# Optimization experiments

Measured on AMD Instinct MI355X. Metric: run time of the kernel, lower is better.

## Reference

```python
import jax, jax.numpy as jnp
import numpy as np

N, E, F_IN = 50000, 800000, 64
H, C1, C2 = 4, 32, 64
NUM_GRAPHS, NUM_CLASSES = 128, 8
NEG_SLOPE = 0.2


def _glorot(key, shape):
    fan_in, fan_out = shape[1], shape[0]
    lim = (6.0 / (fan_in + fan_out)) ** 0.5
    return jax.random.uniform(key, shape, jnp.float32, -lim, lim)


def setup_inputs() -> dict:
    key = jax.random.key(0)
    ks = jax.random.split(key, 20)
    x = jax.random.normal(ks[0], (N, F_IN), jnp.float32)
    edge_index = jax.random.randint(ks[1], (2, E), 0, N, jnp.int64)
    batch = jnp.sort(jax.random.randint(ks[2], (N,), 0, NUM_GRAPHS, jnp.int64))
    d1, d2 = H * C1, H * C2
    return {
        "x": x, "edge_index": edge_index, "batch": batch,
        # GATv2 layer 1 (F_IN -> 32, 4 heads)
        "Wl1": _glorot(ks[3], (d1, F_IN)), "bl1": jnp.zeros((d1,), jnp.float32),
        "Wr1": _glorot(ks[4], (d1, F_IN)), "br1": jnp.zeros((d1,), jnp.float32),
        "att1": _glorot(ks[5], (H, C1)), "bias1": jnp.zeros((d1,), jnp.float32),
        # GATv2 layer 2 (128 -> 64, 4 heads)
        "Wl2": _glorot(ks[6], (d2, d1)), "bl2": jnp.zeros((d2,), jnp.float32),
        "Wr2": _glorot(ks[7], (d2, d1)), "br2": jnp.zeros((d2,), jnp.float32),
        "att2": _glorot(ks[8], (H, C2)), "bias2": jnp.zeros((d2,), jnp.float32),
        # classifier: Linear(256,128) -> ReLU -> (Dropout eval=id) -> Linear(128,8)
        "Wf1": _glorot(ks[9], (128, d2)), "bf1": jnp.zeros((128,), jnp.float32),
        "Wf2": _glorot(ks[10], (NUM_CLASSES, 128)), "bf2": jnp.zeros((NUM_CLASSES,), jnp.float32),
    }


def _gatv2(x, src, dst, Wl, bl, Wr, br, att, bias, heads, out_ch):
    # PyG GATv2Conv: xl = lin_l(x) (source), xr = lin_r(x) (target)
    xl = (x @ Wl.T + bl).reshape(N, heads, out_ch)
    xr = (x @ Wr.T + br).reshape(N, heads, out_ch)
    # per-edge score: att . LeakyReLU(xl[j] + xr[i])  -> [E', H]
    e = jnp.sum(jax.nn.leaky_relu(xl[src] + xr[dst], NEG_SLOPE) * att, axis=-1)
    # destination-grouped softmax (self-loops guarantee every node has an edge)
    emax = jax.ops.segment_max(e, dst, num_segments=N)
    ex = jnp.exp(e - emax[dst])
    denom = jax.ops.segment_sum(ex, dst, num_segments=N)
    alpha = ex / denom[dst]  # [E', H]
    out = jax.ops.segment_sum(alpha[:, :, None] * xl[src], dst, num_segments=N)
    return out.reshape(N, heads * out_ch) + bias


def reference(x, edge_index, batch, Wl1, bl1, Wr1, br1, att1, bias1,
              Wl2, bl2, Wr2, br2, att2, bias2, Wf1, bf1, Wf2, bf2):
    # add self loops (PyG default add_self_loops=True)
    loops = jnp.arange(N, dtype=edge_index.dtype)
    src = jnp.concatenate([edge_index[0], loops])
    dst = jnp.concatenate([edge_index[1], loops])
    h = jax.nn.elu(_gatv2(x, src, dst, Wl1, bl1, Wr1, br1, att1, bias1, H, C1))
    h = jax.nn.elu(_gatv2(h, src, dst, Wl2, bl2, Wr2, br2, att2, bias2, H, C2))
    # global mean pool over graphs
    sums = jax.ops.segment_sum(h, batch, num_segments=NUM_GRAPHS)
    cnts = jax.ops.segment_sum(jnp.ones((N,), h.dtype), batch, num_segments=NUM_GRAPHS)
    pooled = sums / jnp.maximum(cnts, 1.0)[:, None]  # [G, 256]
    # classifier (dropout inactive at inference)
    z = jax.nn.relu(pooled @ Wf1.T + bf1)
    return z @ Wf2.T + bf2
```

## Files before the change

kernel.cpp:

```cpp
#include <hip/hip_runtime.h>
#include <hip/hip_bf16.h>
#include <math.h>

#define NN 50000
#define NE 800000
#define NEP (NE + NN)
#define NG 128
#define PSPLIT 16
#define NSB ((NN + 255) / 256)

typedef unsigned short u16;
typedef __bf16 bf16x8 __attribute__((ext_vector_type(8)));
typedef float f32x4 __attribute__((ext_vector_type(4)));

#define L2E 1.4426950408889634f

__device__ __forceinline__ float eluf(float v) {
  return v > 0.0f ? v : expm1f(v);
}
__device__ __forceinline__ float bflo(unsigned u) {
  union { unsigned i; float f; } c; c.i = u << 16; return c.f;
}
__device__ __forceinline__ float bfhi(unsigned u) {
  union { unsigned i; float f; } c; c.i = u & 0xffff0000u; return c.f;
}
__device__ __forceinline__ bf16x8 load8(const u16* p) {
  union { uint4 u; bf16x8 v; } c;
  c.u = *(const uint4*)p;
  return c.v;
}

__global__ __launch_bounds__(256) void k_deg(const int* __restrict__ ei, int* __restrict__ deg) {
  int t = blockIdx.x * 256 + threadIdx.x;
  if (t >= NEP) return;
  int dst = (t < NE) ? ei[NE + t] : (t - NE);
  atomicAdd(&deg[dst], 1);
}

__global__ __launch_bounds__(256) void k_scan1(const int* __restrict__ deg, int* __restrict__ bsum) {
  __shared__ int red[256];
  int i = blockIdx.x * 256 + threadIdx.x;
  red[threadIdx.x] = (i < NN) ? deg[i] : 0;
  __syncthreads();
  for (int off = 128; off > 0; off >>= 1) {
    if (threadIdx.x < off) red[threadIdx.x] += red[threadIdx.x + off];
    __syncthreads();
  }
  if (threadIdx.x == 0) bsum[blockIdx.x] = red[0];
}

__global__ __launch_bounds__(256) void k_scan2(int* __restrict__ bsum) {
  __shared__ int s[256];
  int t = threadIdx.x;
  s[t] = (t < NSB) ? bsum[t] : 0;
  __syncthreads();
  for (int off = 1; off < 256; off <<= 1) {
    int v = (t >= off) ? s[t - off] : 0;
    __syncthreads();
    s[t] += v;
    __syncthreads();
  }
  if (t < NSB) bsum[t] = (t == 0) ? 0 : s[t - 1];
}

__global__ __launch_bounds__(256) void k_scan3(const int* __restrict__ deg, const int* __restrict__ bsum,
                                               int* __restrict__ rowptr) {
  __shared__ int s[256];
  int t = threadIdx.x;
  int i = blockIdx.x * 256 + t;
  s[t] = (i < NN) ? deg[i] : 0;
  __syncthreads();
  for (int off = 1; off < 256; off <<= 1) {
    int v = (t >= off) ? s[t - off] : 0;
    __syncthreads();
    s[t] += v;
    __syncthreads();
  }
  int excl = (t == 0) ? 0 : s[t - 1];
  if (i <= NN) rowptr[i] = bsum[blockIdx.x] + excl;
}

__global__ __launch_bounds__(256) void k_scatter(const int* __restrict__ ei, const int* __restrict__ rowptr,
                                                 int* __restrict__ fill, int* __restrict__ srcidx) {
  int t = blockIdx.x * 256 + threadIdx.x;
  if (t >= NEP) return;
  int src, dst;
  if (t < NE) { src = ei[t]; dst = ei[NE + t]; } else { src = t - NE; dst = src; }
  int pos = atomicAdd(&fill[dst], 1);
  srcidx[rowptr[dst] + pos] = src;
}

__global__ __launch_bounds__(256) void k_cvtw(const float* __restrict__ w1, const float* __restrict__ w2,
                                              const float* __restrict__ w3, const float* __restrict__ w4,
                                              u16* __restrict__ o) {
  int t = blockIdx.x * 256 + threadIdx.x;
  if (t >= 81920) return;
  float v;
  if (t < 8192) v = w1[t];
  else if (t < 16384) v = w2[t - 8192];
  else if (t < 49152) v = w3[t - 16384];
  else v = w4[t - 49152];
  __hip_bfloat16 b = __float2bfloat16(v);
  o[t] = *(u16*)&b;
}

template <int K, bool AF32>
__global__ __launch_bounds__(256) void k_mfma(const void* __restrict__ Xin,
                                              const u16* __restrict__ Wlb, const u16* __restrict__ Wrb,
                                              const float* __restrict__ bl, const float* __restrict__ br,
                                              __hip_bfloat16* __restrict__ Yl, float* __restrict__ Yr,
                                              int dout) {
  int lane = threadIdx.x & 63;
  int wid = threadIdx.x >> 6;
  int r0 = blockIdx.x * 64 + wid * 16;
  int c0 = blockIdx.y * 64;
  bool isR = (blockIdx.z != 0);
  const u16* W = isR ? Wrb : Wlb;
  const float* bias = isR ? br : bl;

  int arow = min(r0 + (lane & 15), NN - 1);
  int koff = (lane >> 4) * 8;
  const u16*   aph = (const u16*)Xin + (size_t)arow * K + koff;
  const float* apf = (const float*)Xin + (size_t)arow * K + koff;
  const u16* bp = W + (size_t)(c0 + (lane & 15)) * K + koff;

  f32x4 acc[4] = {};
#pragma unroll
  for (int ks = 0; ks < K / 32; ++ks) {
    bf16x8 a;
    if constexpr (AF32) {
      float4 f0 = ((const float4*)(apf + ks * 32))[0];
      float4 f1 = ((const float4*)(apf + ks * 32))[1];
      a[0] = (__bf16)f0.x; a[1] = (__bf16)f0.y; a[2] = (__bf16)f0.z; a[3] = (__bf16)f0.w;
      a[4] = (__bf16)f1.x; a[5] = (__bf16)f1.y; a[6] = (__bf16)f1.z; a[7] = (__bf16)f1.w;
    } else {
      a = load8(aph + ks * 32);
    }
    bf16x8 b0 = load8(bp + ks * 32);
    bf16x8 b1 = load8(bp + 16 * K + ks * 32);
    bf16x8 b2 = load8(bp + 32 * K + ks * 32);
    bf16x8 b3 = load8(bp + 48 * K + ks * 32);
    acc[0] = __builtin_amdgcn_mfma_f32_16x16x32_bf16(a, b0, acc[0], 0, 0, 0);
    acc[1] = __builtin_amdgcn_mfma_f32_16x16x32_bf16(a, b1, acc[1], 0, 0, 0);
    acc[2] = __builtin_amdgcn_mfma_f32_16x16x32_bf16(a, b2, acc[2], 0, 0, 0);
    acc[3] = __builtin_amdgcn_mfma_f32_16x16x32_bf16(a, b3, acc[3], 0, 0, 0);
  }

  int orow = r0 + ((lane >> 4) << 2);
  int ocol = c0 + (lane & 15);
#pragma unroll
  for (int t = 0; t < 4; ++t) {
    int col = ocol + t * 16;
    float bv = bias[col];
    if (!isR) {
#pragma unroll
      for (int v = 0; v < 4; ++v) {
        int row = orow + v;
        if (row < NN) Yl[(size_t)row * dout + col] = __float2bfloat16(acc[t][v] + bv);
      }
    } else {
#pragma unroll
      for (int v = 0; v < 4; ++v) {
        int row = orow + v;
        if (row < NN) Yr[(size_t)row * dout + col] = acc[t][v] + bv;
      }
    }
  }
}

template <int D, bool OBF16>
__global__ __launch_bounds__(256) void k_fused(const int* __restrict__ rowptr, const int* __restrict__ srcidx,
                                               const u16* __restrict__ xl, const float* __restrict__ xr,
                                               const float* __restrict__ att, const float* __restrict__ bias,
                                               void* __restrict__ outv) {
  constexpr int V = D / 64;
  constexpr int SH = (V == 2) ? 8 : 9;
  int lane = threadIdx.x & 63;
  int node = blockIdx.x * 4 + (threadIdx.x >> 6);
  if (node >= NN) return;
  int lo = rowptr[node], hi = rowptr[node + 1];

  float xrv[V], attv[V];
  float rlin = 0.f;
#pragma unroll
  for (int q = 0; q < V; ++q) {
    attv[q] = att[lane * V + q] * (0.4f * L2E);
    xrv[q]  = xr[(size_t)node * D + lane * V + q];
    rlin = fmaf(attv[q], xrv[q], rlin);
  }
#pragma unroll
  for (int off = 1; off < 16; off <<= 1) rlin += __shfl_xor(rlin, off);
  float S0 = 1.5f * rlin;

  const char* xb = (const char*)xl;
  unsigned lb = (unsigned)lane << (SH - 6);

  float denom = 0.f;
  float acc[V] = {};

  auto gather = [&](int j, float* xv) {
    unsigned off = ((unsigned)j << SH) + lb;
    if constexpr (V == 2) {
      unsigned u = *(const unsigned*)(xb + off);
      xv[0] = bflo(u); xv[1] = bfhi(u);
    } else {
      uint2 u = *(const uint2*)(xb + off);
      xv[0] = bflo(u.x); xv[1] = bfhi(u.x);
      xv[2] = bflo(u.y); xv[3] = bfhi(u.y);
    }
  };
  auto score2 = [&](const float* xv) {
    float pa = 0.f, pl = 0.f;
#pragma unroll
    for (int q = 0; q < V; ++q) {
      float u = xv[q] + xrv[q];
      pa = fmaf(attv[q], fabsf(u), pa);
      pl = fmaf(attv[q], xv[q], pl);
    }
    return fmaf(pl, 1.5f, pa);
  };
  auto update = [&](float p, const float* xv) {
    float w = exp2f(p + S0);
    denom += w;
#pragma unroll
    for (int q = 0; q < V; ++q) acc[q] = fmaf(w, xv[q], acc[q]);
  };

  int s = lo;
  for (; s + 3 < hi; s += 4) {
    int j0 = srcidx[s], j1 = srcidx[s + 1], j2 = srcidx[s + 2], j3 = srcidx[s + 3];
    float xv0[V], xv1[V], xv2[V], xv3[V];
    gather(j0, xv0); gather(j1, xv1); gather(j2, xv2); gather(j3, xv3);
    float p0 = score2(xv0);
    float p1 = score2(xv1);
    float p2 = score2(xv2);
    float p3 = score2(xv3);
#pragma unroll
    for (int off = 1; off < 16; off <<= 1) {
      p0 += __shfl_xor(p0, off);
      p1 += __shfl_xor(p1, off);
      p2 += __shfl_xor(p2, off);
      p3 += __shfl_xor(p3, off);
    }
    update(p0, xv0); update(p1, xv1); update(p2, xv2); update(p3, xv3);
  }
  for (; s < hi; ++s) {
    int j0 = srcidx[s];
    float xv0[V];
    gather(j0, xv0);
    float p0 = score2(xv0);
#pragma unroll
    for (int off = 1; off < 16; off <<= 1) p0 += __shfl_xor(p0, off);
    update(p0, xv0);
  }

  float rd = 1.0f / denom;
  float vals[V];
#pragma unroll
  for (int q = 0; q < V; ++q) vals[q] = eluf(fmaf(acc[q], rd, bias[lane * V + q]));

  if constexpr (OBF16) {
    __hip_bfloat16 tmp[V];
#pragma unroll
    for (int q = 0; q < V; ++q) tmp[q] = __float2bfloat16(vals[q]);
    if constexpr (V == 2) ((unsigned*)outv)[(size_t)node * (D / 2) + lane] = *(unsigned*)tmp;
    else                  ((uint2*)outv)[(size_t)node * (D / 4) + lane] = *(uint2*)tmp;
  } else {
    if constexpr (V == 2) {
      float2 f = {vals[0], vals[1]};
      ((float2*)outv)[(size_t)node * (D / 2) + lane] = f;
    } else {
      float4 f = {vals[0], vals[1], vals[2], vals[3]};
      ((float4*)outv)[(size_t)node * (D / 4) + lane] = f;
    }
  }
}

__device__ __forceinline__ int lowerb(const int* __restrict__ a, int n, int v) {
  int lo = 0, hi = n;
  while (lo < hi) { int mid = (lo + hi) >> 1; if (a[mid] < v) lo = mid + 1; else hi = mid; }
  return lo;
}

__global__ __launch_bounds__(256) void k_pool(const float* __restrict__ h2, const int* __restrict__ batch,
                                              float* __restrict__ pooled_p) {
  int g = blockIdx.x, sp = blockIdx.y, t = threadIdx.x;
  __shared__ int sh[2];
  if (t < 2) sh[t] = lowerb(batch, NN, g + t);
  __syncthreads();
  int lo = sh[0], hi = sh[1];
  int cnt = hi - lo;
  int chunk = (cnt + PSPLIT - 1) / PSPLIT;
  int b = lo + sp * chunk;
  int e = min(b + chunk, hi);
  float acc = 0.f;
  for (int n = b; n < e; ++n) acc += h2[(size_t)n * 256 + t];
  pooled_p[((size_t)g * PSPLIT + sp) * 256 + t] = acc;
}

__global__ __launch_bounds__(128) void k_cls(const float* __restrict__ pooled_p, const int* __restrict__ batch,
                                             const float* __restrict__ Wf1, const float* __restrict__ bf1,
                                             const float* __restrict__ Wf2, const float* __restrict__ bf2,
                                             float* __restrict__ out) {
  __shared__ float p[256];
  __shared__ float z[128];
  __shared__ int sh[2];
  int g = blockIdx.x, t = threadIdx.x;
  if (t < 2) sh[t] = lowerb(batch, NN, g + t);
  __syncthreads();
  float cnt = (float)(sh[1] - sh[0]);
  float rinv = 1.0f / fmaxf(cnt, 1.0f);
  const float* pp = pooled_p + (size_t)g * PSPLIT * 256;
#pragma unroll 1
  for (int c = t; c < 256; c += 128) {
    float s = 0.f;
#pragma unroll
    for (int sp = 0; sp < PSPLIT; ++sp) s += pp[sp * 256 + c];
    p[c] = s * rinv;
  }
  __syncthreads();
  float a = bf1[t];
  const float* wr = Wf1 + (size_t)t * 256;
  for (int k = 0; k < 256; ++k) a += p[k] * wr[k];
  z[t] = fmaxf(a, 0.f);
  __syncthreads();
  if (t < 8) {
    float o = bf2[t];
    const float* w2 = Wf2 + t * 128;
    for (int k = 0; k < 128; ++k) o += z[k] * w2[k];
    out[g * 8 + t] = o;
  }
}

extern "C" void kernel_launch(void* const* d_in, const int* in_sizes, int n_in,
                              void* d_out, int out_size, void* d_ws, size_t ws_size,
                              hipStream_t stream) {
  const float* x     = (const float*)d_in[0];
  const int*   ei    = (const int*)d_in[1];
  const int*   batch = (const int*)d_in[2];
  const float* Wl1 = (const float*)d_in[3];
  const float* bl1 = (const float*)d_in[4];
  const float* Wr1 = (const float*)d_in[5];
  const float* br1 = (const float*)d_in[6];
  const float* att1  = (const float*)d_in[7];
  const float* bias1 = (const float*)d_in[8];
  const float* Wl2 = (const float*)d_in[9];
  const float* bl2 = (const float*)d_in[10];
  const float* Wr2 = (const float*)d_in[11];
  const float* br2 = (const float*)d_in[12];
  const float* att2  = (const float*)d_in[13];
  const float* bias2 = (const float*)d_in[14];
  const float* Wf1 = (const float*)d_in[15];
  const float* bf1 = (const float*)d_in[16];
  const float* Wf2 = (const float*)d_in[17];
  const float* bf2 = (const float*)d_in[18];
  float* out = (float*)d_out;

  char* w = (char*)d_ws;
  size_t off = 0;
  auto alloc = [&](size_t bytes) -> void* {
    void* p = w + off;
    off += (bytes + 255) & ~(size_t)255;
    return p;
  };
  int* rowptr = (int*)alloc((NN + 1) * sizeof(int));
  int* deg    = (int*)alloc(NN * sizeof(int));
  int* fill   = (int*)alloc(NN * sizeof(int));
  int* bsum   = (int*)alloc(NSB * sizeof(int));
  int* srcidx = (int*)alloc((size_t)NEP * sizeof(int));
  u16* Wb     = (u16*)alloc((size_t)81920 * sizeof(u16));
  u16* Wl1b = Wb, *Wr1b = Wb + 8192, *Wl2b = Wb + 16384, *Wr2b = Wb + 49152;
  char* regA  = (char*)alloc((size_t)NN * 128 * 2 + (size_t)NN * 128 * 4);
  __hip_bfloat16* xl1 = (__hip_bfloat16*)regA;
  float*          xr1 = (float*)(regA + (size_t)NN * 128 * 2);
  __hip_bfloat16* xl2 = (__hip_bfloat16*)regA;
  u16*   h1b    = (u16*)alloc((size_t)NN * 128 * sizeof(u16));
  float* xr2    = (float*)alloc((size_t)NN * 256 * sizeof(float));
  float* h2     = xr2;
  float* pooled_p = (float*)alloc((size_t)NG * PSPLIT * 256 * sizeof(float));
  (void)ws_size; (void)in_sizes; (void)n_in; (void)out_size;

  hipMemsetAsync(deg, 0, NN * sizeof(int), stream);
  hipMemsetAsync(fill, 0, NN * sizeof(int), stream);

  const int EB = (NEP + 255) / 256;
  k_deg<<<EB, 256, 0, stream>>>(ei, deg);
  k_scan1<<<NSB, 256, 0, stream>>>(deg, bsum);
  k_scan2<<<1, 256, 0, stream>>>(bsum);
  k_scan3<<<NSB, 256, 0, stream>>>(deg, bsum, rowptr);
  k_scatter<<<EB, 256, 0, stream>>>(ei, rowptr, fill, srcidx);

  k_cvtw<<<(81920 + 255) / 256, 256, 0, stream>>>(Wl1, Wr1, Wl2, Wr2, Wb);

  const int RB = (NN + 63) / 64;
  dim3 g1(RB, 2, 2);
  k_mfma<64, true><<<g1, 256, 0, stream>>>(x, Wl1b, Wr1b, bl1, br1, xl1, xr1, 128);
  k_fused<128, true><<<(NN + 3) / 4, 256, 0, stream>>>(rowptr, srcidx, (const u16*)xl1, xr1,
                                                       att1, bias1, h1b);

  dim3 g2(RB, 4, 2);
  k_mfma<128, false><<<g2, 256, 0, stream>>>(h1b, Wl2b, Wr2b, bl2, br2, xl2, xr2, 256);
  k_fused<256, false><<<(NN + 3) / 4, 256, 0, stream>>>(rowptr, srcidx, (const u16*)xl2, xr2,
                                                        att2, bias2, h2);

  dim3 gp(NG, PSPLIT);
  k_pool<<<gp, 256, 0, stream>>>(h2, batch, pooled_p);
  k_cls<<<NG, 128, 0, stream>>>(pooled_p, batch, Wf1, bf1, Wf2, bf2, out);
}
```

Measured before the change: 347.9 us.

## Specialize layer-1 aggregation kernel to process two edges per wavefront

Adds a dedicated layer-1 GATv2 aggregation kernel where each 64-lane wavefront splits into two 32-lane halves, each handling a different edge with 4 channels per lane. This doubles edge-level parallelism for the 128-wide feature dimension and unrolls four edges per iteration, so more independent gathers are in flight. The two halves' partial sums are combined at the end with a cross-half shuffle. It keeps the non-max-subtracted exp2 softmax with a precomputed offset, which assumes scores stay bounded.

Measured after the change: 345.8 us (median of 2 runs). No clear change (-0.6%).

```diff
diff --git a/kernel.cpp b/kernel.cpp
--- a/kernel.cpp
+++ b/kernel.cpp
@@ -165,6 +165,100 @@
         if (row < NN) Yr[(size_t)row * dout + col] = acc[t][v] + bv;
       }
     }
+  }
+}
+
+__global__ __launch_bounds__(256) void k_fused1(const int* __restrict__ rowptr, const int* __restrict__ srcidx,
+                                                const u16* __restrict__ xl, const float* __restrict__ xr,
+                                                const float* __restrict__ att, const float* __restrict__ bias,
+                                                u16* __restrict__ outv) {
+  int lane = threadIdx.x & 63;
+  int node = blockIdx.x * 4 + (threadIdx.x >> 6);
+  if (node >= NN) return;
+  int il = lane & 31, sub = lane >> 5;
+  int lo = rowptr[node], hi = rowptr[node + 1];
+
+  float xrv[4], attv[4];
+  float rlin = 0.f;
+#pragma unroll
+  for (int q = 0; q < 4; ++q) {
+    attv[q] = att[il * 4 + q] * (0.4f * L2E);
+    xrv[q]  = xr[(size_t)node * 128 + il * 4 + q];
+    rlin = fmaf(attv[q], xrv[q], rlin);
+  }
+#pragma unroll
+  for (int off = 1; off < 8; off <<= 1) rlin += __shfl_xor(rlin, off);
+  float S0 = 1.5f * rlin;
+
+  const char* xb = (const char*)xl;
+  unsigned lb = (unsigned)il << 3;
+
+  float denom = 0.f;
+  float acc[4] = {};
+
+  auto gather = [&](int j, float* xv) {
+    uint2 u = *(const uint2*)(xb + (((unsigned)j << 8) + lb));
+    xv[0] = bflo(u.x); xv[1] = bfhi(u.x);
+    xv[2] = bflo(u.y); xv[3] = bfhi(u.y);
+  };
+  auto score2 = [&](const float* xv) {
+    float pa = 0.f, pl = 0.f;
+#pragma unroll
+    for (int q = 0; q < 4; ++q) {
+      float u = xv[q] + xrv[q];
+      pa = fmaf(attv[q], fabsf(u), pa);
+      pl = fmaf(attv[q], xv[q], pl);
+    }
+    return fmaf(pl, 1.5f, pa);
+  };
+  auto update = [&](float p, const float* xv) {
+    float w = exp2f(p + S0);
+    denom += w;
+#pragma unroll
+    for (int q = 0; q < 4; ++q) acc[q] = fmaf(w, xv[q], acc[q]);
+  };
+
+  int s = lo;
+  for (; s + 3 < hi; s += 4) {
+    int j0 = srcidx[s + sub];
+    int j1 = srcidx[s + 2 + sub];
+    float xv0[4], xv1[4];
+    gather(j0, xv0); gather(j1, xv1);
+    float p0 = score2(xv0);
+    float p1 = score2(xv1);
+#pragma unroll
+    for (int off = 1; off < 8; off <<= 1) {
+      p0 += __shfl_xor(p0, off);
+      p1 += __shfl_xor(p1, off);
+    }
+    update(p0, xv0); update(p1, xv1);
+  }
+  for (; s < hi; s += 2) {
+    int e = s + sub;
+    bool valid = e < hi;
+    int j = srcidx[valid ? e : lo];
+    float xv[4];
+    gather(j, xv);
+    float p = score2(xv);
+#pragma unroll
+    for (int off = 1; off < 8; off <<= 1) p += __shfl_xor(p, off);
+    float w = valid ? exp2f(p + S0) : 0.f;
+    denom += w;
+#pragma unroll
+    for (int q = 0; q < 4; ++q) acc[q] = fmaf(w, xv[q], acc[q]);
+  }
+
+  denom += __shfl_xor(denom, 32);
+#pragma unroll
+  for (int q = 0; q < 4; ++q) acc[q] += __shfl_xor(acc[q], 32);
+
+  if (sub == 0) {
+    float rd = 1.0f / denom;
+    __hip_bfloat16 tmp[4];
+#pragma unroll
+    for (int q = 0; q < 4; ++q)
+      tmp[q] = __float2bfloat16(eluf(fmaf(acc[q], rd, bias[il * 4 + q])));
+    ((uint2*)outv)[(size_t)node * 32 + il] = *(uint2*)tmp;
   }
 }
 
@@ -395,8 +489,8 @@
   const int RB = (NN + 63) / 64;
   dim3 g1(RB, 2, 2);
   k_mfma<64, true><<<g1, 256, 0, stream>>>(x, Wl1b, Wr1b, bl1, br1, xl1, xr1, 128);
-  k_fused<128, true><<<(NN + 3) / 4, 256, 0, stream>>>(rowptr, srcidx, (const u16*)xl1, xr1,
-                                                       att1, bias1, h1b);
+  k_fused1<<<(NN + 3) / 4, 256, 0, stream>>>(rowptr, srcidx, (const u16*)xl1, xr1,
+                                             att1, bias1, h1b);
 
   dim3 g2(RB, 4, 2);
   k_mfma<128, false><<<g2, 256, 0, stream>>>(h1b, Wl2b, Wr2b, bl2, br2, xl2, xr2, 256);
```
